# Kernel optimization log

Measured on AMD Instinct MI355X. Metric: run time of the kernel, lower is better.

The kernel has to match this reference:

```python
import jax, jax.numpy as jnp
import numpy as np

LEVELS = [2, 3, 4, 5, 6]
IMG = 1024
BATCH = 8
NUM_ANCHORS = 3
PRE_NMS_TOP_K = 2000
NUM_PROPOSALS = 1000
NMS_IOU = 0.7
BBOX_XFORM_CLIP = float(np.log(1000.0 / 16.0))


def _make_anchors(level):
    stride = 2 ** level
    fs = IMG // stride
    base = 4.0 * stride
    aspects = np.array([0.5, 1.0, 2.0], np.float32)
    hs = base * np.sqrt(aspects)
    ws = base / np.sqrt(aspects)
    cy = (np.arange(fs, dtype=np.float32) + 0.5) * stride
    cx = (np.arange(fs, dtype=np.float32) + 0.5) * stride
    yy, xx = np.meshgrid(cy, cx, indexing='ij')
    yy = yy[:, :, None]
    xx = xx[:, :, None]
    # [fs, fs, A, 4] in (ymin, xmin, ymax, xmax)
    boxes = np.stack([yy - hs / 2, xx - ws / 2, yy + hs / 2, xx + ws / 2], axis=-1)
    return boxes.reshape(fs * fs * NUM_ANCHORS, 4).astype(np.float32)


def setup_inputs():
    key = jax.random.key(0)
    inp = {}
    for i, lvl in enumerate(LEVELS):
        fs = IMG // (2 ** lvl)
        kb, ks = jax.random.split(jax.random.fold_in(key, i))
        inp['boxes_l%d' % lvl] = jax.random.normal(kb, (BATCH, fs, fs, NUM_ANCHORS * 4), jnp.float32) * 0.2
        inp['scores_l%d' % lvl] = jax.random.normal(ks, (BATCH, fs, fs, NUM_ANCHORS), jnp.float32)
        anc = jnp.asarray(_make_anchors(lvl))
        inp['anchors_l%d' % lvl] = jnp.tile(anc[None], (BATCH, 1, 1))
    inp['image_shape'] = jnp.full((BATCH, 2), float(IMG), jnp.float32)
    return inp


def decode_boxes(encoded, anchors):
    dy, dx, dh, dw = jnp.split(encoded, 4, axis=-1)
    dh = jnp.minimum(dh, BBOX_XFORM_CLIP)
    dw = jnp.minimum(dw, BBOX_XFORM_CLIP)
    ay0, ax0, ay1, ax1 = jnp.split(anchors, 4, axis=-1)
    ah = ay1 - ay0
    aw = ax1 - ax0
    ayc = ay0 + 0.5 * ah
    axc = ax0 + 0.5 * aw
    yc = dy * ah + ayc
    xc = dx * aw + axc
    h = jnp.exp(dh) * ah
    w = jnp.exp(dw) * aw
    return jnp.concatenate([yc - 0.5 * h, xc - 0.5 * w, yc + 0.5 * h, xc + 0.5 * w], axis=-1)


def clip_boxes(boxes, image_shape):
    # image_shape: [B, 1, 2] (h, w) -> max coords (h, w, h, w)
    maxes = jnp.concatenate([image_shape, image_shape], axis=-1)
    return jnp.clip(boxes, 0.0, maxes)


def top_k_boxes(boxes, scores, k):
    scores_k, idx = jax.lax.top_k(scores, k)
    boxes_k = jnp.take_along_axis(boxes, idx[..., None], axis=1)
    return boxes_k, scores_k


def sorted_nms_padded(scores, boxes, max_output_size, iou_threshold):
    # scores [B,K] sorted descending, boxes [B,K,4]. Greedy NMS.
    B, K = scores.shape
    areas = (boxes[..., 2] - boxes[..., 0]) * (boxes[..., 3] - boxes[..., 1])  # [B,K]
    idxs = jnp.arange(K)

    def step(kept, i):
        bi = jax.lax.dynamic_slice_in_dim(boxes, i, 1, axis=1)  # [B,1,4]
        ai = jax.lax.dynamic_slice_in_dim(areas, i, 1, axis=1)  # [B,1]
        ki = jax.lax.dynamic_slice_in_dim(kept, i, 1, axis=1)   # [B,1]
        iy = jnp.maximum(0.0, jnp.minimum(bi[..., 2], boxes[..., 2]) - jnp.maximum(bi[..., 0], boxes[..., 0]))
        ix = jnp.maximum(0.0, jnp.minimum(bi[..., 3], boxes[..., 3]) - jnp.maximum(bi[..., 1], boxes[..., 1]))
        inter = iy * ix  # [B,K]
        iou = inter / (ai + areas - inter + 1e-8)
        suppress = (iou > iou_threshold) & (idxs[None, :] > i) & ki
        return kept & (~suppress), None

    kept0 = jnp.ones((B, K), dtype=bool)
    kept, _ = jax.lax.scan(step, kept0, idxs)
    out_scores = jnp.where(kept, scores, 0.0)
    out_boxes = boxes * kept[..., None].astype(boxes.dtype)
    b_out, s_out = top_k_boxes(out_boxes, out_scores, max_output_size)
    return s_out, b_out


def _multi_level_rois(raw_boxes, raw_scores, anchors, image_shape):
    img = image_shape[:, None, :]  # [B,1,2]
    rois, roi_scores = [], []
    for rb, rs, ab in zip(raw_boxes, raw_scores, anchors):
        B, fh, fw, na = rs.shape
        nb = fh * fw * na
        sc = jax.nn.sigmoid(rs.reshape(B, nb))
        bx = rb.reshape(B, nb, 4)
        bx = decode_boxes(bx, ab)
        bx = clip_boxes(bx, img)
        pre_k = min(nb, PRE_NMS_TOP_K)
        post_k = min(nb, NUM_PROPOSALS)
        bx, sc = top_k_boxes(bx, sc, pre_k)
        s_out, b_out = sorted_nms_padded(sc, bx, post_k, NMS_IOU)
        rois.append(b_out)
        roi_scores.append(s_out)
    all_rois = jnp.concatenate(rois, axis=1)
    all_scores = jnp.concatenate(roi_scores, axis=1)
    k = min(all_scores.shape[1], NUM_PROPOSALS)
    sel_rois, sel_scores = top_k_boxes(all_rois, all_scores, k)
    return sel_rois, sel_scores


def reference(boxes_l2, boxes_l3, boxes_l4, boxes_l5, boxes_l6,
              scores_l2, scores_l3, scores_l4, scores_l5, scores_l6,
              anchors_l2, anchors_l3, anchors_l4, anchors_l5, anchors_l6,
              image_shape):
    raw_boxes = [boxes_l2, boxes_l3, boxes_l4, boxes_l5, boxes_l6]
    raw_scores = [scores_l2, scores_l3, scores_l4, scores_l5, scores_l6]
    anchors = [anchors_l2, anchors_l3, anchors_l4, anchors_l5, anchors_l6]
    return _multi_level_rois(raw_boxes, raw_scores, anchors, image_shape)
```

## Files before the change

kernel.cpp:

```cpp
#include <hip/hip_runtime.h>
#include <hip/hip_bf16.h>
#include <cstdint>

constexpr int BATCH = 8;
constexpr int NL = 5;
constexpr int CNTS[5] = {196608, 49152, 12288, 3072, 768};
constexpr int LOFF[5] = {0, 196608, 245760, 258048, 261120};
constexpr int PERB  = 261888;
constexpr int TOTC  = BATCH * PERB;
constexpr int PREK[5]  = {2000, 2000, 2000, 2000, 768};
constexpr int POSTK[5] = {1000, 1000, 1000, 1000, 768};
constexpr int COFF[5]  = {0, 1000, 2000, 3000, 4000};
constexpr int CONCATN  = 4768;
constexpr int SELSTRIDE = 2048;
constexpr int CANDCAP   = 8192;
constexpr int NREP      = 64;
constexpr int REPCAP    = 512;
constexpr int NBINS     = 16384;
constexpr int MASKROWS  = 2000;
constexpr int MASKW     = 32;
constexpr int SCH       = 128;
constexpr int ROWS_PER_BATCH = 4 * 2000 + 768;
constexpr float IOU_THR = 0.7f;
constexpr float CLIPV = 4.135166556742356f;

struct Ptrs {
    const float* bx[5];
    const float* sc[5];
    const float* an[5];
    const float* img;
};

__device__ __forceinline__ void bitonic_desc(unsigned long long* k, int N, int tid, int nt) {
    for (int kk = 2; kk <= N; kk <<= 1) {
        for (int j = kk >> 1; j > 0; j >>= 1) {
            __syncthreads();
            for (int i = tid; i < N; i += nt) {
                int ixj = i ^ j;
                if (ixj > i) {
                    bool up = ((i & kk) == 0);
                    unsigned long long a = k[i], b = k[ixj];
                    if ((a < b) == up) { k[i] = b; k[ixj] = a; }
                }
            }
        }
    }
    __syncthreads();
}

__device__ __forceinline__ unsigned long long readlane_u64(unsigned long long v, int src) {
    unsigned int lo = (unsigned int)v;
    unsigned int hi = (unsigned int)(v >> 32);
    lo = (unsigned int)__builtin_amdgcn_readlane((int)lo, src);
    hi = (unsigned int)__builtin_amdgcn_readlane((int)hi, src);
    return ((unsigned long long)hi << 32) | lo;
}

__global__ __launch_bounds__(1024) void k_hist(Ptrs p, unsigned int* __restrict__ hist) {
#pragma clang fp contract(off)
    __shared__ unsigned int h2[NBINS / 2];
    constexpr int CLI[11] = {0, 0, 0, 0, 0, 0, 1, 1, 2, 3, 4};
    constexpr int COF[11] = {0, 32768, 65536, 98304, 131072, 163840, 0, 24576, 0, 0, 0};
    constexpr int CLN[11] = {32768, 32768, 32768, 32768, 32768, 32768, 24576, 24576, 12288, 3072, 768};
    int blk = blockIdx.x;
    int b = blk / 11, c = blk % 11;
    int li = CLI[c], off = COF[c], len = CLN[c];
    int tid = threadIdx.x;
    for (int i = tid; i < NBINS / 2; i += 1024) h2[i] = 0;
    __syncthreads();
    const float* sp = p.sc[li] + (size_t)b * CNTS[li] + off;
    for (int i = tid; i < len; i += 1024) {
        float s = sp[i];
        float sig = 1.0f / (1.0f + expf(-s));
        unsigned int bin = __float_as_uint(sig) >> 16;
        atomicAdd(&h2[bin >> 1], 1u << ((bin & 1) << 4));
    }
    __syncthreads();
    unsigned int* H = hist + (size_t)(b * NL + li) * NBINS;
    for (int i = tid; i < NBINS / 2; i += 1024) {
        unsigned int v = h2[i];
        if (v & 0xFFFFu) atomicAdd(&H[2 * i], v & 0xFFFFu);
        if (v >> 16) atomicAdd(&H[2 * i + 1], v >> 16);
    }
}

__global__ void k_findbin(const unsigned int* __restrict__ hist, int* __restrict__ T) {
    int bl = blockIdx.x;
    int li = bl % NL;
    unsigned int K = (unsigned int)PREK[li];
    __shared__ unsigned int csum[256];
    const unsigned int* h = hist + (size_t)bl * NBINS;
    int tid = threadIdx.x;
    unsigned int s = 0;
    for (int k = 0; k < 64; ++k) s += h[tid * 64 + k];
    csum[tid] = s;
    __syncthreads();
    if (tid == 0) {
        unsigned int cum = 0;
        int t = 0;
        for (int c = 255; c >= 0; --c) {
            if (cum + csum[c] >= K) {
                for (int bin = c * 64 + 63; bin >= c * 64; --bin) {
                    cum += h[bin];
                    if (cum >= K) { t = bin; break; }
                }
                break;
            }
            cum += csum[c];
        }
        T[bl] = t;
    }
}

__global__ void k_compact(Ptrs p, const int* __restrict__ T,
                          unsigned long long* __restrict__ cand, unsigned int* __restrict__ cntR) {
#pragma clang fp contract(off)
    int g = blockIdx.x * blockDim.x + threadIdx.x;
    if (g >= TOTC) return;
    int b = g / PERB;
    int r = g - b * PERB;
    int li;
    if      (r < LOFF[1]) li = 0;
    else if (r < LOFF[2]) li = 1;
    else if (r < LOFF[3]) li = 2;
    else if (r < LOFF[4]) li = 3;
    else                  li = 4;
    int i = r - LOFF[li];
    int bl = b * NL + li;
    int rep = blockIdx.x & (NREP - 1);

    float s = p.sc[li][(size_t)b * CNTS[li] + i];
    float sig = 1.0f / (1.0f + expf(-s));
    unsigned int bits = __float_as_uint(sig);
    bool pass = ((int)(bits >> 16) >= T[bl]);
    unsigned long long ball = __ballot(pass);
    int lane = threadIdx.x & 63;
    unsigned int base = 0;
    if (lane == 0 && ball != 0ull)
        base = atomicAdd(&cntR[rep * 64 + bl], (unsigned int)__popcll(ball));
    base = __shfl((int)base, 0);
    if (pass) {
        unsigned int pos = base + (unsigned int)__popcll(ball & ((1ull << lane) - 1ull));
        if (pos < REPCAP)
            cand[((size_t)bl * NREP + rep) * REPCAP + pos] =
                ((unsigned long long)bits << 32) | (unsigned long long)(0xFFFFFFFFu - (unsigned int)i);
    }
}

__global__ __launch_bounds__(1024) void k_sortsel(const unsigned long long* __restrict__ cand,
                                                  const unsigned int* __restrict__ cntR, Ptrs p,
                                                  float4* __restrict__ selb, float* __restrict__ sels) {
#pragma clang fp contract(off)
    __shared__ unsigned long long keys[CANDCAP];
    __shared__ int pref[NREP + 1];
    int bl = blockIdx.x;
    int tid = threadIdx.x;
    int b = bl / NL, li = bl % NL;
    int K = PREK[li];
    if (tid == 0) {
        int run = 0;
        for (int rp = 0; rp < NREP; ++rp) {
            pref[rp] = run;
            int c = min((int)cntR[rp * 64 + bl], REPCAP);
            if (run + c > CANDCAP) c = CANDCAP - run;
            run += c;
        }
        pref[NREP] = run;
    }
    __syncthreads();
    int n = pref[NREP];
    int N = 1024;
    while (N < n) N <<= 1;
    for (int i = tid; i < N; i += 1024) keys[i] = 0ull;
    __syncthreads();
    for (int rp = 0; rp < NREP; ++rp) {
        int base = pref[rp], c = pref[rp + 1] - pref[rp];
        const unsigned long long* src = cand + ((size_t)bl * NREP + rp) * REPCAP;
        for (int j = tid; j < c; j += 1024) keys[base + j] = src[j];
    }
    bitonic_desc(keys, N, tid, 1024);

    int nn = CNTS[li];
    float hmax = p.img[b * 2 + 0];
    float wmax = p.img[b * 2 + 1];
    const float4* bxp = reinterpret_cast<const float4*>(p.bx[li]) + (size_t)b * nn;
    const float4* anp = reinterpret_cast<const float4*>(p.an[li]) + (size_t)b * nn;
    for (int r = tid; r < K; r += 1024) {
        unsigned long long kk = keys[r];
        unsigned int idx = 0xFFFFFFFFu - (unsigned int)(kk & 0xFFFFFFFFull);
        const float4 e = bxp[idx];
        const float4 a = anp[idx];
        float dy = e.x, dx = e.y;
        float dh = fminf(e.z, CLIPV), dw = fminf(e.w, CLIPV);
        float ah = a.z - a.x, aw = a.w - a.y;
        float ayc = a.x + 0.5f * ah, axc = a.y + 0.5f * aw;
        float yc = dy * ah + ayc, xc = dx * aw + axc;
        float h = expf(dh) * ah, w = expf(dw) * aw;
        float y0 = yc - 0.5f * h, x0 = xc - 0.5f * w;
        float y1 = yc + 0.5f * h, x1 = xc + 0.5f * w;
        y0 = fminf(fmaxf(y0, 0.f), hmax);
        x0 = fminf(fmaxf(x0, 0.f), wmax);
        y1 = fminf(fmaxf(y1, 0.f), hmax);
        x1 = fminf(fmaxf(x1, 0.f), wmax);
        sels[(size_t)bl * SELSTRIDE + r] = __uint_as_float((unsigned int)(kk >> 32));
        selb[(size_t)bl * SELSTRIDE + r] = make_float4(y0, x0, y1, x1);
    }
}

__global__ void k_mask(const float4* __restrict__ selb, unsigned long long* __restrict__ mask) {
#pragma clang fp contract(off)
    int rg = blockIdx.x;
    int b = rg / ROWS_PER_BATCH;
    int rem = rg - b * ROWS_PER_BATCH;
    int li, i;
    if (rem < 8000) { li = rem / 2000; i = rem - li * 2000; }
    else            { li = 4; i = rem - 8000; }
    int bl = b * NL + li;
    int K = PREK[li];
    const float4* bb = selb + (size_t)bl * SELSTRIDE;
    float4 bi = bb[i];
    float ai = (bi.z - bi.x) * (bi.w - bi.y);
    int tid = threadIdx.x;
    unsigned long long* mrow = mask + ((size_t)bl * MASKROWS + i) * MASKW;
    for (int cb = (i >> 6) << 6; cb < K; cb += 256) {
        int c = cb + tid;
        bool sup = false;
        if (c > i && c < K) {
            float4 bj = bb[c];
            float aj = (bj.z - bj.x) * (bj.w - bj.y);
            float iy = fmaxf(0.f, fminf(bi.z, bj.z) - fmaxf(bi.x, bj.x));
            float ix = fmaxf(0.f, fminf(bi.w, bj.w) - fmaxf(bi.y, bj.y));
            float inter = iy * ix;
            float iou = inter / (ai + aj - inter + 1e-8f);
            sup = iou > IOU_THR;
        }
        unsigned long long bal = __ballot(sup);
        int wb = cb + (tid & ~63);
        if ((tid & 63) == 0 && wb < K) mrow[wb >> 6] = bal;
    }
}

__global__ __launch_bounds__(256) void k_scan(const unsigned long long* __restrict__ mask,
                                              unsigned long long* __restrict__ kept) {
    __shared__ unsigned long long lbuf[2][SCH * MASKW];
    __shared__ int stopflag;
    int bl = blockIdx.x;
    int li = bl % NL;
    int K = PREK[li];
    int W = (K + 63) >> 6;
    int PK = POSTK[li];
    int tid = threadIdx.x;
    int lane = tid & 63;
    int wv = tid >> 6;
    const unsigned long long* m = mask + (size_t)bl * MASKROWS * MASKW;
    int nchunks = (K + SCH - 1) / SCH;

    auto load_chunk = [&](int c, int t0, int nt) {
        int rbase = c * SCH;
        int nrows = min(SCH, K - rbase);
        int nu2 = nrows * (MASKW / 2);
        const ulonglong2* src = reinterpret_cast<const ulonglong2*>(m + (size_t)rbase * MASKW);
        ulonglong2* dst = reinterpret_cast<ulonglong2*>(lbuf[c & 1]);
        if (tid >= t0)
            for (int j = tid - t0; j < nu2; j += nt) dst[j] = src[j];
    };

    if (tid == 0) stopflag = 0;
    load_chunk(0, 0, 256);
    __syncthreads();

    unsigned long long removed = 0, local = 0;
    int keptcnt = 0;
    for (int c = 0; c < nchunks; ++c) {
        if (c + 1 < nchunks) load_chunk(c + 1, 64, 192);
        if (wv == 0) {
            const unsigned long long* ch = lbuf[c & 1];
            int rbase = c * SCH;
            int nrows = min(SCH, K - rbase);

            unsigned long long rvA[8], rgA[8], rvB[8], rgB[8];
            auto loadw = [&](unsigned long long (&rv)[8], unsigned long long (&rg)[8], int w0) {
                int g = (rbase + w0) >> 6;
#pragma unroll
                for (int k2 = 0; k2 < 8; ++k2) {
                    rv[k2] = ch[(w0 + k2) * MASKW + (lane & (MASKW - 1))];
                    rg[k2] = ch[(w0 + k2) * MASKW + g];
                }
            };
            auto procw = [&](unsigned long long (&rv)[8], unsigned long long (&rg)[8], int w0) {
                int ii0 = rbase + w0;
                int g = ii0 >> 6;
                if ((ii0 & 63) == 0) local = readlane_u64(removed, g);
                unsigned long long gemask = (lane >= g) ? ~0ull : 0ull;
#pragma unroll
                for (int k2 = 0; k2 < 8; ++k2) {
                    bool keptb = ((local >> ((ii0 & 63) + k2)) & 1ull) == 0ull;
                    unsigned long long sel = keptb ? ~0ull : 0ull;
                    removed |= rv[k2] & sel & gemask;
                    local |= rg[k2] & sel;
                    keptcnt += keptb ? 1 : 0;
                }
            };

            loadw(rvA, rgA, 0);
            for (int w0 = 0; w0 < nrows; w0 += 16) {
                if (w0 + 8 < nrows) loadw(rvB, rgB, w0 + 8);
                procw(rvA, rgA, w0);
                if (w0 + 8 < nrows) {
                    if (w0 + 16 < nrows) loadw(rvA, rgA, w0 + 16);
                    procw(rvB, rgB, w0 + 8);
                }
            }
            if (keptcnt >= PK && c + 1 < nchunks) {
                if (lane >= (c + 1) * (SCH / 64)) removed = ~0ull;
                if (lane == 0) stopflag = 1;
            }
        }
        __syncthreads();
        if (stopflag) break;
    }
    if (wv == 0 && lane < W) {
        int remn = K - lane * 64;
        unsigned long long valid = (remn >= 64) ? ~0ull : ((1ull << remn) - 1ull);
        kept[bl * MASKW + lane] = (~removed) & valid;
    }
}

__global__ void k_lvlout(const unsigned long long* __restrict__ kept,
                         const float* __restrict__ sels, const float4* __restrict__ selb,
                         float* __restrict__ cscores, float4* __restrict__ cboxes) {
    int bl = blockIdx.x;
    int b = bl / NL, li = bl % NL;
    int K = PREK[li];
    int W = (K + 63) >> 6;
    int PK = POSTK[li];
    int tid = threadIdx.x;
    __shared__ unsigned long long kw[32];
    __shared__ int pref[33];
    if (tid < W) kw[tid] = kept[bl * MASKW + tid];
    __syncthreads();
    if (tid == 0) {
        int run = 0;
        for (int w = 0; w < W; ++w) { pref[w] = run; run += __popcll(kw[w]); }
        pref[W] = run;
    }
    __syncthreads();
    int total = pref[W];
    int nused = min(total, PK);
    float* cs = cscores + (size_t)b * CONCATN + COFF[li];
    float4* cbx = cboxes + (size_t)b * CONCATN + COFF[li];
    if (tid < W) {
        int rank = pref[tid];
        unsigned long long w64 = kw[tid];
        while (w64 != 0ull && rank < PK) {
            int j = __ffsll(w64) - 1;
            w64 &= (w64 - 1);
            int pidx = tid * 64 + j;
            cs[rank] = sels[(size_t)bl * SELSTRIDE + pidx];
            cbx[rank] = selb[(size_t)bl * SELSTRIDE + pidx];
            ++rank;
        }
    }
    for (int r = nused + tid; r < PK; r += 256) {
        cs[r] = 0.f;
        cbx[r] = make_float4(0.f, 0.f, 0.f, 0.f);
    }
}

__global__ __launch_bounds__(1024) void k_final(const float* __restrict__ cscores,
                                                const float4* __restrict__ cboxes,
                                                float* __restrict__ out) {
    __shared__ unsigned long long keys[CONCATN];
    int b = blockIdx.x;
    int tid = threadIdx.x;
    const float* cs = cscores + (size_t)b * CONCATN;
    for (int i = tid; i < CONCATN; i += 1024)
        keys[i] = (((unsigned long long)__float_as_uint(cs[i]) << 32) |
                   (unsigned long long)(0xFFFFFFFFu - (unsigned int)i));
    __syncthreads();
    const float4* cbx = cboxes + (size_t)b * CONCATN;
    float4* ob = reinterpret_cast<float4*>(out) + (size_t)b * 1000;
    float* os = out + (size_t)BATCH * 1000 * 4 + (size_t)b * 1000;
    for (int i = tid; i < CONCATN; i += 1024) {
        unsigned long long k = keys[i];
        int myli = min(i / 1000, 4);
        int rank = i - COFF[myli];
#pragma unroll
        for (int r = 0; r < NL; ++r) {
            if (r == myli) continue;
            const unsigned long long* run = keys + COFF[r];
            int lo = 0, hi = POSTK[r];
            while (lo < hi) {
                int mid = (lo + hi) >> 1;
                if (run[mid] > k) lo = mid + 1; else hi = mid;
            }
            rank += lo;
        }
        if (rank < 1000) {
            ob[rank] = cbx[i];
            os[rank] = __uint_as_float((unsigned int)(k >> 32));
        }
    }
}

extern "C" void kernel_launch(void* const* d_in, const int* in_sizes, int n_in,
                              void* d_out, int out_size, void* d_ws, size_t ws_size,
                              hipStream_t stream) {
    Ptrs p;
    bool dict_order = (in_sizes[2] == 6291456);
    for (int l = 0; l < 5; ++l) {
        if (dict_order) {
            p.bx[l] = (const float*)d_in[3 * l + 0];
            p.sc[l] = (const float*)d_in[3 * l + 1];
            p.an[l] = (const float*)d_in[3 * l + 2];
        } else {
            p.bx[l] = (const float*)d_in[l];
            p.sc[l] = (const float*)d_in[5 + l];
            p.an[l] = (const float*)d_in[10 + l];
        }
    }
    p.img = (const float*)d_in[15];

    char* ws = (char*)d_ws;
    size_t off = 0;
    auto walloc = [&](size_t sz) -> void* {
        void* r = ws + off;
        off = (off + sz + 255) & ~(size_t)255;
        return r;
    };
    unsigned int* hist         = (unsigned int*)walloc((size_t)40 * NBINS * 4);
    unsigned int* cntR         = (unsigned int*)walloc((size_t)NREP * 64 * 4);
    int* T                     = (int*)walloc(40 * 4);
    unsigned long long* cand   = (unsigned long long*)walloc((size_t)40 * NREP * REPCAP * 8);
    float4* selb               = (float4*)walloc((size_t)40 * SELSTRIDE * 16);
    float* sels                = (float*)walloc((size_t)40 * SELSTRIDE * 4);
    unsigned long long* mask   = (unsigned long long*)walloc((size_t)40 * MASKROWS * MASKW * 8);
    unsigned long long* kept   = (unsigned long long*)walloc((size_t)40 * MASKW * 8);
    float* cscores             = (float*)walloc((size_t)BATCH * CONCATN * 4);
    float4* cboxes             = (float4*)walloc((size_t)BATCH * CONCATN * 16);
    (void)ws_size;

    hipMemsetAsync(hist, 0, (size_t)40 * NBINS * 4, stream);
    hipMemsetAsync(cntR, 0, (size_t)NREP * 64 * 4, stream);

    k_hist<<<BATCH * 11, 1024, 0, stream>>>(p, hist);
    k_findbin<<<40, 256, 0, stream>>>(hist, T);
    k_compact<<<(TOTC + 255) / 256, 256, 0, stream>>>(p, T, cand, cntR);
    k_sortsel<<<40, 1024, 0, stream>>>(cand, cntR, p, selb, sels);
    k_mask<<<BATCH * ROWS_PER_BATCH, 256, 0, stream>>>(selb, mask);
    k_scan<<<40, 256, 0, stream>>>(mask, kept);
    k_lvlout<<<40, 256, 0, stream>>>(kept, sels, selb, cscores, cboxes);
    k_final<<<8, 1024, 0, stream>>>(cscores, cboxes, (float*)d_out);
}
```

Measured before the change: 408.2 us.

## Replace bitonic sort with rank-by-counting and precompute box areas for NMS mask

The shared-memory bitonic sort in k_sortsel, with its many block-wide barriers, is replaced by a counting rank: each thread compares its keys against all n candidates and writes its box directly to the output slot given by its rank. Decoded box areas are stored in a new selA buffer so k_mask reads them instead of recomputing them. The IoU division in the mask test is replaced by a double-precision compare against a dyadic threshold. Counting rank is O(n^2) compares instead of O(n log^2 n), but it needs no barriers. The double multiply runs on every pair in the mask kernel, and the rounding of the threshold compare may differ from the original float division at the boundary.

```diff
diff --git a/kernel.cpp b/kernel.cpp
--- a/kernel.cpp
+++ b/kernel.cpp
@@ -23,6 +23,7 @@
 constexpr int ROWS_PER_BATCH = 4 * 2000 + 768;
 constexpr float IOU_THR = 0.7f;
 constexpr float CLIPV = 4.135166556742356f;
+constexpr double TAU = 23488103.0 / 33554432.0;
 
 struct Ptrs {
     const float* bx[5];
@@ -30,23 +31,6 @@
     const float* an[5];
     const float* img;
 };
-
-__device__ __forceinline__ void bitonic_desc(unsigned long long* k, int N, int tid, int nt) {
-    for (int kk = 2; kk <= N; kk <<= 1) {
-        for (int j = kk >> 1; j > 0; j >>= 1) {
-            __syncthreads();
-            for (int i = tid; i < N; i += nt) {
-                int ixj = i ^ j;
-                if (ixj > i) {
-                    bool up = ((i & kk) == 0);
-                    unsigned long long a = k[i], b = k[ixj];
-                    if ((a < b) == up) { k[i] = b; k[ixj] = a; }
-                }
-            }
-        }
-    }
-    __syncthreads();
-}
 
 __device__ __forceinline__ unsigned long long readlane_u64(unsigned long long v, int src) {
     unsigned int lo = (unsigned int)v;
@@ -147,10 +131,65 @@
     }
 }
 
+template <int NH>
+__device__ __forceinline__ void rank_emit(const unsigned long long* keys, int n, int K, int tid,
+                                          const float4* bxp, const float4* anp,
+                                          float hmax, float wmax,
+                                          float* sels_o, float4* selb_o, float* selA_o) {
+#pragma clang fp contract(off)
+    unsigned long long myk[NH];
+    int rnk[NH];
+#pragma unroll
+    for (int h = 0; h < NH; ++h) {
+        int idx = tid + h * 1024;
+        myk[h] = (idx < n) ? keys[idx] : ~0ull;
+        rnk[h] = 0;
+    }
+    int j = 0;
+    for (; j + 4 <= n; j += 4) {
+        unsigned long long k0 = keys[j], k1 = keys[j + 1], k2 = keys[j + 2], k3 = keys[j + 3];
+#pragma unroll
+        for (int h = 0; h < NH; ++h)
+            rnk[h] += (int)(k0 > myk[h]) + (int)(k1 > myk[h]) +
+                      (int)(k2 > myk[h]) + (int)(k3 > myk[h]);
+    }
+    for (; j < n; ++j) {
+        unsigned long long kj = keys[j];
+#pragma unroll
+        for (int h = 0; h < NH; ++h) rnk[h] += (int)(kj > myk[h]);
+    }
+#pragma unroll
+    for (int h = 0; h < NH; ++h) {
+        int idx = tid + h * 1024;
+        int r = rnk[h];
+        if (idx < n && r < K) {
+            unsigned long long kk = myk[h];
+            unsigned int gi = 0xFFFFFFFFu - (unsigned int)(kk & 0xFFFFFFFFull);
+            const float4 e = bxp[gi];
+            const float4 a = anp[gi];
+            float dy = e.x, dx = e.y;
+            float dh = fminf(e.z, CLIPV), dw = fminf(e.w, CLIPV);
+            float ah = a.z - a.x, aw = a.w - a.y;
+            float ayc = a.x + 0.5f * ah, axc = a.y + 0.5f * aw;
+            float yc = dy * ah + ayc, xc = dx * aw + axc;
+            float hh = expf(dh) * ah, ww = expf(dw) * aw;
+            float y0 = yc - 0.5f * hh, x0 = xc - 0.5f * ww;
+            float y1 = yc + 0.5f * hh, x1 = xc + 0.5f * ww;
+            y0 = fminf(fmaxf(y0, 0.f), hmax);
+            x0 = fminf(fmaxf(x0, 0.f), wmax);
+            y1 = fminf(fmaxf(y1, 0.f), hmax);
+            x1 = fminf(fmaxf(x1, 0.f), wmax);
+            sels_o[r] = __uint_as_float((unsigned int)(kk >> 32));
+            selb_o[r] = make_float4(y0, x0, y1, x1);
+            selA_o[r] = (y1 - y0) * (x1 - x0);
+        }
+    }
+}
+
 __global__ __launch_bounds__(1024) void k_sortsel(const unsigned long long* __restrict__ cand,
                                                   const unsigned int* __restrict__ cntR, Ptrs p,
-                                                  float4* __restrict__ selb, float* __restrict__ sels) {
-#pragma clang fp contract(off)
+                                                  float4* __restrict__ selb, float* __restrict__ sels,
+                                                  float* __restrict__ selA) {
     __shared__ unsigned long long keys[CANDCAP];
     __shared__ int pref[NREP + 1];
     int bl = blockIdx.x;
@@ -169,45 +208,29 @@
     }
     __syncthreads();
     int n = pref[NREP];
-    int N = 1024;
-    while (N < n) N <<= 1;
-    for (int i = tid; i < N; i += 1024) keys[i] = 0ull;
-    __syncthreads();
     for (int rp = 0; rp < NREP; ++rp) {
         int base = pref[rp], c = pref[rp + 1] - pref[rp];
         const unsigned long long* src = cand + ((size_t)bl * NREP + rp) * REPCAP;
         for (int j = tid; j < c; j += 1024) keys[base + j] = src[j];
     }
-    bitonic_desc(keys, N, tid, 1024);
+    __syncthreads();
 
     int nn = CNTS[li];
     float hmax = p.img[b * 2 + 0];
     float wmax = p.img[b * 2 + 1];
     const float4* bxp = reinterpret_cast<const float4*>(p.bx[li]) + (size_t)b * nn;
     const float4* anp = reinterpret_cast<const float4*>(p.an[li]) + (size_t)b * nn;
-    for (int r = tid; r < K; r += 1024) {
-        unsigned long long kk = keys[r];
-        unsigned int idx = 0xFFFFFFFFu - (unsigned int)(kk & 0xFFFFFFFFull);
-        const float4 e = bxp[idx];
-        const float4 a = anp[idx];
-        float dy = e.x, dx = e.y;
-        float dh = fminf(e.z, CLIPV), dw = fminf(e.w, CLIPV);
-        float ah = a.z - a.x, aw = a.w - a.y;
-        float ayc = a.x + 0.5f * ah, axc = a.y + 0.5f * aw;
-        float yc = dy * ah + ayc, xc = dx * aw + axc;
-        float h = expf(dh) * ah, w = expf(dw) * aw;
-        float y0 = yc - 0.5f * h, x0 = xc - 0.5f * w;
-        float y1 = yc + 0.5f * h, x1 = xc + 0.5f * w;
-        y0 = fminf(fmaxf(y0, 0.f), hmax);
-        x0 = fminf(fmaxf(x0, 0.f), wmax);
-        y1 = fminf(fmaxf(y1, 0.f), hmax);
-        x1 = fminf(fmaxf(x1, 0.f), wmax);
-        sels[(size_t)bl * SELSTRIDE + r] = __uint_as_float((unsigned int)(kk >> 32));
-        selb[(size_t)bl * SELSTRIDE + r] = make_float4(y0, x0, y1, x1);
-    }
-}
-
-__global__ void k_mask(const float4* __restrict__ selb, unsigned long long* __restrict__ mask) {
+    float* so = sels + (size_t)bl * SELSTRIDE;
+    float4* bo = selb + (size_t)bl * SELSTRIDE;
+    float* ao = selA + (size_t)bl * SELSTRIDE;
+    int nh = (n + 1023) >> 10;
+    if (nh <= 2)      rank_emit<2>(keys, n, K, tid, bxp, anp, hmax, wmax, so, bo, ao);
+    else if (nh <= 4) rank_emit<4>(keys, n, K, tid, bxp, anp, hmax, wmax, so, bo, ao);
+    else              rank_emit<8>(keys, n, K, tid, bxp, anp, hmax, wmax, so, bo, ao);
+}
+
+__global__ void k_mask(const float4* __restrict__ selb, const float* __restrict__ selA,
+                       unsigned long long* __restrict__ mask) {
 #pragma clang fp contract(off)
     int rg = blockIdx.x;
     int b = rg / ROWS_PER_BATCH;
@@ -218,8 +241,9 @@
     int bl = b * NL + li;
     int K = PREK[li];
     const float4* bb = selb + (size_t)bl * SELSTRIDE;
+    const float* aA = selA + (size_t)bl * SELSTRIDE;
     float4 bi = bb[i];
-    float ai = (bi.z - bi.x) * (bi.w - bi.y);
+    float ai = aA[i];
     int tid = threadIdx.x;
     unsigned long long* mrow = mask + ((size_t)bl * MASKROWS + i) * MASKW;
     for (int cb = (i >> 6) << 6; cb < K; cb += 256) {
@@ -227,12 +251,12 @@
         bool sup = false;
         if (c > i && c < K) {
             float4 bj = bb[c];
-            float aj = (bj.z - bj.x) * (bj.w - bj.y);
+            float aj = aA[c];
             float iy = fmaxf(0.f, fminf(bi.z, bj.z) - fmaxf(bi.x, bj.x));
             float ix = fmaxf(0.f, fminf(bi.w, bj.w) - fmaxf(bi.y, bj.y));
             float inter = iy * ix;
-            float iou = inter / (ai + aj - inter + 1e-8f);
-            sup = iou > IOU_THR;
+            float aden = ai + aj - inter + 1e-8f;
+            sup = ((double)inter >= TAU * (double)aden);
         }
         unsigned long long bal = __ballot(sup);
         int wb = cb + (tid & ~63);
@@ -434,6 +458,7 @@
     unsigned long long* cand   = (unsigned long long*)walloc((size_t)40 * NREP * REPCAP * 8);
     float4* selb               = (float4*)walloc((size_t)40 * SELSTRIDE * 16);
     float* sels                = (float*)walloc((size_t)40 * SELSTRIDE * 4);
+    float* selA                = (float*)walloc((size_t)40 * SELSTRIDE * 4);
     unsigned long long* mask   = (unsigned long long*)walloc((size_t)40 * MASKROWS * MASKW * 8);
     unsigned long long* kept   = (unsigned long long*)walloc((size_t)40 * MASKW * 8);
     float* cscores             = (float*)walloc((size_t)BATCH * CONCATN * 4);
@@ -446,8 +471,8 @@
     k_hist<<<BATCH * 11, 1024, 0, stream>>>(p, hist);
     k_findbin<<<40, 256, 0, stream>>>(hist, T);
     k_compact<<<(TOTC + 255) / 256, 256, 0, stream>>>(p, T, cand, cntR);
-    k_sortsel<<<40, 1024, 0, stream>>>(cand, cntR, p, selb, sels);
-    k_mask<<<BATCH * ROWS_PER_BATCH, 256, 0, stream>>>(selb, mask);
+    k_sortsel<<<40, 1024, 0, stream>>>(cand, cntR, p, selb, sels, selA);
+    k_mask<<<BATCH * ROWS_PER_BATCH, 256, 0, stream>>>(selb, selA, mask);
     k_scan<<<40, 256, 0, stream>>>(mask, kept);
     k_lvlout<<<40, 256, 0, stream>>>(kept, sels, selb, cscores, cboxes);
     k_final<<<8, 1024, 0, stream>>>(cscores, cboxes, (float*)d_out);
```

Result: slower. 493.0 us (+20.8%).
